# Optimization experiments

Measured on AMD Instinct MI355X. Metric: run time of the kernel, lower is better.

## Reference

```python
import math
import jax, jax.numpy as jnp
import numpy as np

B, S, H, NH = 4, 2048, 1024, 16
HD = H // NH
SCALE = math.sqrt(H)  # module divides by sqrt(hidden_dim), not sqrt(head_dim)


def setup_inputs() -> dict:
    key = jax.random.key(0)
    ks = jax.random.split(key, 9)
    lim = 1.0 / math.sqrt(H)
    def lin(kw, kb):
        W = jax.random.uniform(kw, (H, H), jnp.float32, -lim, lim)
        b = jax.random.uniform(kb, (H,), jnp.float32, -lim, lim)
        return W, b
    Wq, bq = lin(ks[0], ks[1])
    Wk, bk = lin(ks[2], ks[3])
    Wv, bv = lin(ks[4], ks[5])
    Wo, bo = lin(ks[6], ks[7])
    hidden_states = jax.random.normal(ks[8], (B, S, H), jnp.float32)
    masks = jnp.ones((B, S), jnp.float32)
    return {"hidden_states": hidden_states, "masks": masks,
            "Wq": Wq, "bq": bq, "Wk": Wk, "bk": bk,
            "Wv": Wv, "bv": bv, "Wo": Wo, "bo": bo}


def reference(hidden_states, masks, Wq, bq, Wk, bk, Wv, bv, Wo, bo):
    bsz, msl, hdim = hidden_states.shape
    def proj(W, b):
        # [b, s, h] -> [b, nh, s, hd]
        y = hidden_states @ W.T + b
        return y.reshape(bsz, msl, NH, HD).transpose(0, 2, 1, 3)
    q = proj(Wq, bq)
    k = proj(Wk, bk)
    v = proj(Wv, bv)
    scores = jnp.einsum('bnqd,bnkd->bnqk', q, k) / SCALE
    # mask outer product: [b,1,q,k], zero where either token is padded
    m2 = (masks[:, None, :, None] * masks[:, None, None, :])
    scores = jnp.where(m2 == 0, jnp.float32(-1e12), scores)
    attn = jax.nn.softmax(scores, axis=-1)
    ctx = jnp.einsum('bnqk,bnkd->bnqd', attn, v)
    ctx = ctx.transpose(0, 2, 1, 3).reshape(bsz, msl, hdim)
    return ctx @ Wo.T + bo
```

## Files before the change

kernel.cpp:

```cpp
#include <hip/hip_runtime.h>
#include <hip/hip_bf16.h>
#include <stdint.h>

typedef unsigned short u16;
typedef __attribute__((ext_vector_type(4))) float f32x4;
typedef __attribute__((ext_vector_type(8))) short bf16x8;
typedef __attribute__((ext_vector_type(4))) unsigned int u32x4;

#define GLL16(src, dst) __builtin_amdgcn_global_load_lds( \
    (const __attribute__((address_space(1))) void*)(src), \
    (__attribute__((address_space(3))) void*)(dst), 16, 0, 0)

static __device__ __forceinline__ u16 f2bf(float x) {
    uint32_t u = __builtin_bit_cast(uint32_t, x);
    u += 0x7fffu + ((u >> 16) & 1u);
    return (u16)(u >> 16);
}

static __device__ __forceinline__ uint32_t cvtpk(float lo, float hi) {
    uint32_t r;
    asm("v_cvt_pk_bf16_f32 %0, %1, %2" : "=v"(r) : "v"(lo), "v"(hi));
    return r;
}

__global__ __launch_bounds__(256) void cvt_f32_bf16(
        const float* __restrict__ in, u16* __restrict__ out, int n4) {
    int i = blockIdx.x * 256 + threadIdx.x;
    if (i >= n4) return;
    float4 v = ((const float4*)in)[i];
    ushort4 o;
    o.x = f2bf(v.x); o.y = f2bf(v.y); o.z = f2bf(v.z); o.w = f2bf(v.w);
    ((ushort4*)out)[i] = o;
}

__global__ __launch_bounds__(256) void cvt_w4(
        const float* __restrict__ s0, const float* __restrict__ s1,
        const float* __restrict__ s2, const float* __restrict__ s3,
        u16* __restrict__ dst) {
    int wsel = blockIdx.y;
    const float* s = (wsel == 0) ? s0 : (wsel == 1) ? s1 : (wsel == 2) ? s2 : s3;
    int i = blockIdx.x * 256 + threadIdx.x;
    float4 v = ((const float4*)s)[i];
    ushort4 o;
    o.x = f2bf(v.x); o.y = f2bf(v.y); o.z = f2bf(v.z); o.w = f2bf(v.w);
    ((ushort4*)(dst + (size_t)wsel * 1024 * 1024))[i] = o;
}

__global__ __launch_bounds__(256, 2) void gemm_qkv(
        const u16* __restrict__ A, const u16* __restrict__ W,
        const float* __restrict__ bq, const float* __restrict__ bk,
        const float* __restrict__ bv,
        u16* __restrict__ Qo, u16* __restrict__ Ko, u16* __restrict__ Vo) {
    __shared__ __align__(16) u16 As[2][128 * 32];
    __shared__ __align__(16) u16 Bs[2][128 * 32];
    const int tid = threadIdx.x;
    const int lane = tid & 63;
    const int w = tid >> 6, wm = w >> 1, wn = w & 1;
    const int l15 = lane & 15, l4 = lane >> 4;
    int v = (blockIdx.x & 7) * 192 + (blockIdx.x >> 3);
    int vy = v / 24, vx = v - vy * 24;
    const int m0 = vy * 128, n0 = vx * 128;
    const float SC2 = 0.03125f * 1.44269504088896f;

    f32x4 acc[4][4];
#pragma unroll
    for (int i = 0; i < 4; i++)
#pragma unroll
        for (int j = 0; j < 4; j++) acc[i][j] = f32x4{0.f, 0.f, 0.f, 0.f};

#define QKV_STAGE(buf, kt) do {                                            \
    _Pragma("unroll")                                                      \
    for (int i_ = 0; i_ < 2; i_++) {                                       \
        int c_ = tid + i_ * 256;                                           \
        int row_ = c_ >> 2, slot_ = c_ & 3;                                \
        int cc_ = slot_ ^ ((row_ >> 1) & 3);                               \
        GLL16(A + (size_t)(m0 + row_) * 1024 + (kt) + cc_ * 8, As[buf] + c_ * 8); \
    }                                                                      \
    _Pragma("unroll")                                                      \
    for (int i_ = 0; i_ < 2; i_++) {                                       \
        int c_ = tid + i_ * 256;                                           \
        int row_ = c_ >> 2, slot_ = c_ & 3;                                \
        int cc_ = slot_ ^ ((row_ >> 1) & 3);                               \
        GLL16(W + (size_t)(n0 + row_) * 1024 + (kt) + cc_ * 8, Bs[buf] + c_ * 8); \
    }                                                                      \
} while (0)

    QKV_STAGE(0, 0);
    __syncthreads();

    for (int kt = 0; kt < 1024; kt += 32) {
        const int cur = (kt >> 5) & 1;
        if (kt != 992) QKV_STAGE(cur ^ 1, kt + 32);

        bf16x8 af[4], bfr[4];
#pragma unroll
        for (int i = 0; i < 4; i++) {
            int row = wm * 64 + i * 16 + l15;
            int slot = l4 ^ ((row >> 1) & 3);
            af[i] = *(const bf16x8*)(As[cur] + row * 32 + slot * 8);
        }
#pragma unroll
        for (int j = 0; j < 4; j++) {
            int row = wn * 64 + j * 16 + l15;
            int slot = l4 ^ ((row >> 1) & 3);
            bfr[j] = *(const bf16x8*)(Bs[cur] + row * 32 + slot * 8);
        }
#pragma unroll
        for (int i = 0; i < 4; i++)
#pragma unroll
            for (int j = 0; j < 4; j++)
                acc[i][j] = __builtin_amdgcn_mfma_f32_16x16x32_bf16(af[i], bfr[j], acc[i][j], 0, 0, 0);
        __syncthreads();
    }
#undef QKV_STAGE

#pragma unroll
    for (int j = 0; j < 4; j++) {
        int col = n0 + wn * 64 + j * 16 + l15;
        int sel = col >> 10;
        float bvv = (sel == 0) ? bq[col] : (sel == 1) ? bk[col - 1024] : bv[col - 2048];
#pragma unroll
        for (int i = 0; i < 4; i++) {
            int rowb = m0 + wm * 64 + i * 16 + l4 * 4;
            if (sel == 0) {
#pragma unroll
                for (int r = 0; r < 4; r++)
                    Qo[(size_t)(rowb + r) * 1024 + col] = f2bf((acc[i][j][r] + bvv) * SC2);
            } else if (sel == 1) {
#pragma unroll
                for (int r = 0; r < 4; r++)
                    Ko[(size_t)(rowb + r) * 1024 + (col - 1024)] = f2bf(acc[i][j][r] + bvv);
            } else {
                int cc = col - 2048;
                int bb = rowb >> 11;
                int sp = ((m0 + wm * 64) & 2047) + (i >> 1) * 32 + l4 * 8 + (i & 1) * 4;
                int hh = cc >> 6, dd = cc & 63;
                ushort4 o;
                o.x = f2bf(acc[i][j][0] + bvv);
                o.y = f2bf(acc[i][j][1] + bvv);
                o.z = f2bf(acc[i][j][2] + bvv);
                o.w = f2bf(acc[i][j][3] + bvv);
                *(ushort4*)(Vo + ((size_t)((bb * 16 + hh) * 64 + dd)) * 2048 + sp) = o;
            }
        }
    }
}

__global__ __launch_bounds__(256, 2) void gemm_o(
        const u16* __restrict__ A, const u16* __restrict__ W,
        const float* __restrict__ bias, float* __restrict__ out) {
    __shared__ __align__(16) u16 As[2][128 * 32];
    __shared__ __align__(16) u16 Bs[2][128 * 32];
    const int tid = threadIdx.x;
    const int lane = tid & 63;
    const int w = tid >> 6, wm = w >> 1, wn = w & 1;
    const int l15 = lane & 15, l4 = lane >> 4;
    int v = (blockIdx.x & 7) * 64 + (blockIdx.x >> 3);
    int vy = v >> 3, vx = v & 7;
    const int m0 = vy * 128, n0 = vx * 128;

    f32x4 acc[4][4];
#pragma unroll
    for (int i = 0; i < 4; i++)
#pragma unroll
        for (int j = 0; j < 4; j++) acc[i][j] = f32x4{0.f, 0.f, 0.f, 0.f};

#define O_STAGE(buf, kt) do {                                              \
    _Pragma("unroll")                                                      \
    for (int i_ = 0; i_ < 2; i_++) {                                       \
        int c_ = tid + i_ * 256;                                           \
        int row_ = c_ >> 2, slot_ = c_ & 3;                                \
        int cc_ = slot_ ^ ((row_ >> 1) & 3);                               \
        GLL16(A + (size_t)(m0 + row_) * 1024 + (kt) + cc_ * 8, As[buf] + c_ * 8); \
    }                                                                      \
    _Pragma("unroll")                                                      \
    for (int i_ = 0; i_ < 2; i_++) {                                       \
        int c_ = tid + i_ * 256;                                           \
        int row_ = c_ >> 2, slot_ = c_ & 3;                                \
        int cc_ = slot_ ^ ((row_ >> 1) & 3);                               \
        GLL16(W + (size_t)(n0 + row_) * 1024 + (kt) + cc_ * 8, Bs[buf] + c_ * 8); \
    }                                                                      \
} while (0)

    O_STAGE(0, 0);
    __syncthreads();

    for (int kt = 0; kt < 1024; kt += 32) {
        const int cur = (kt >> 5) & 1;
        if (kt != 992) O_STAGE(cur ^ 1, kt + 32);

        bf16x8 af[4], bfr[4];
#pragma unroll
        for (int i = 0; i < 4; i++) {
            int row = wm * 64 + i * 16 + l15;
            int slot = l4 ^ ((row >> 1) & 3);
            af[i] = *(const bf16x8*)(As[cur] + row * 32 + slot * 8);
        }
#pragma unroll
        for (int j = 0; j < 4; j++) {
            int row = wn * 64 + j * 16 + l15;
            int slot = l4 ^ ((row >> 1) & 3);
            bfr[j] = *(const bf16x8*)(Bs[cur] + row * 32 + slot * 8);
        }
#pragma unroll
        for (int i = 0; i < 4; i++)
#pragma unroll
            for (int j = 0; j < 4; j++)
                acc[i][j] = __builtin_amdgcn_mfma_f32_16x16x32_bf16(af[i], bfr[j], acc[i][j], 0, 0, 0);
        __syncthreads();
    }
#undef O_STAGE

#pragma unroll
    for (int j = 0; j < 4; j++) {
        int col = n0 + wn * 64 + j * 16 + l15;
        float bvv = bias[col];
#pragma unroll
        for (int i = 0; i < 4; i++) {
            int rowb = m0 + wm * 64 + i * 16 + l4 * 4;
#pragma unroll
            for (int r = 0; r < 4; r++)
                out[(size_t)(rowb + r) * 1024 + col] = acc[i][j][r] + bvv;
        }
    }
}

__global__ __launch_bounds__(256, 3) void attn_fused(
        const u16* __restrict__ Q, const u16* __restrict__ K,
        const u16* __restrict__ Vt, const float* __restrict__ mask,
        u16* __restrict__ ctx) {
    __shared__ __align__(16) u16 Ks[2][64 * 64];
    __shared__ __align__(16) u16 Vs[2][64 * 64];

    const int tid = threadIdx.x, lane = tid & 63, w = tid >> 6;
    const int l15 = lane & 15, l4 = lane >> 4;
    const int bid = blockIdx.x;
    const int inner = bid >> 3;
    const int bh = ((inner >> 4) << 3) | (bid & 7);
    const int b = bh >> 4, h = bh & 15;
    const int qw = (inner & 15) * 128 + w * 32;
    const float THR2 = 8.0f;

    const u16* Qg = Q + (size_t)b * 2048 * 1024 + h * 64;
    const u16* Kg = K + (size_t)b * 2048 * 1024 + h * 64;
    const u16* Vg = Vt + (size_t)bh * 64 * 2048;
    const float* mp = mask + b * 2048;

    bool anym;
    {
        bool bad = false;
#pragma unroll
        for (int i = 0; i < 8; i++) {
            float4 a = ((const float4*)mp)[lane * 8 + i];
            bad |= (a.x == 0.f) | (a.y == 0.f) | (a.z == 0.f) | (a.w == 0.f);
        }
        anym = (__ballot(bad) != 0ull);
    }

#define STAGE_KV(buf, kvbase) do {                                         \
    _Pragma("unroll")                                                      \
    for (int i_ = 0; i_ < 2; i_++) {                                       \
        int c_ = tid + i_ * 256;                                           \
        int row_ = c_ >> 3, slot_ = c_ & 7;                                \
        int cc_ = slot_ ^ (row_ & 7);                                      \
        GLL16(Kg + (size_t)((kvbase) + row_) * 1024 + cc_ * 8, Ks[buf] + c_ * 8); \
    }                                                                      \
    _Pragma("unroll")                                                      \
    for (int i_ = 0; i_ < 2; i_++) {                                       \
        int c_ = tid + i_ * 256;                                           \
        int row_ = c_ >> 3, slot_ = c_ & 7;                                \
        int cc_ = slot_ ^ (row_ & 7);                                      \
        GLL16(Vg + (size_t)row_ * 2048 + (kvbase) + cc_ * 8, Vs[buf] + c_ * 8); \
    }                                                                      \
} while (0)

    bf16x8 qfr[2][2];
#pragma unroll
    for (int qi = 0; qi < 2; qi++)
#pragma unroll
        for (int kf = 0; kf < 2; kf++)
            qfr[qi][kf] = *(const bf16x8*)(Qg + (size_t)(qw + qi * 16 + l15) * 1024 + kf * 32 + l4 * 8);

    float mq01[2];
#pragma unroll
    for (int qi = 0; qi < 2; qi++)
        mq01[qi] = (mp[qw + qi * 16 + l15] != 0.f) ? 1.f : 0.f;

    float m_run[2] = {0.f, 0.f};
    f32x4 acc_l[2];
    f32x4 oaccT[4][2];
#pragma unroll
    for (int qi = 0; qi < 2; qi++) acc_l[qi] = f32x4{0.f, 0.f, 0.f, 0.f};
#pragma unroll
    for (int df = 0; df < 4; df++)
#pragma unroll
        for (int qi = 0; qi < 2; qi++) oaccT[df][qi] = f32x4{0.f, 0.f, 0.f, 0.f};

    const u32x4 ones4 = u32x4{0x3F803F80u, 0x3F803F80u, 0x3F803F80u, 0x3F803F80u};
    const bf16x8 ones = __builtin_bit_cast(bf16x8, ones4);

    STAGE_KV(0, 0);

    for (int it = 0; it < 32; ++it) {
        const int cur = it & 1;
        const int kv0 = it * 64;

        if (it != 31) {
            STAGE_KV(cur ^ 1, kv0 + 64);
            asm volatile("s_waitcnt vmcnt(4)" ::: "memory");
        } else {
            asm volatile("s_waitcnt vmcnt(0)" ::: "memory");
        }
        __builtin_amdgcn_s_barrier();

        bf16x8 kfr[4][2];
#pragma unroll
        for (int kvf = 0; kvf < 4; kvf++)
#pragma unroll
            for (int kf = 0; kf < 2; kf++) {
                int row = kvf * 16 + l15;
                int slot = (kf * 4 + l4) ^ (row & 7);
                kfr[kvf][kf] = *(const bf16x8*)(Ks[cur] + row * 64 + slot * 8);
            }
        f32x4 p[4][2];
#pragma unroll
        for (int kvf = 0; kvf < 4; kvf++)
#pragma unroll
            for (int qi = 0; qi < 2; qi++) p[kvf][qi] = f32x4{0.f, 0.f, 0.f, 0.f};
        __builtin_amdgcn_s_setprio(1);
#pragma unroll
        for (int kvf = 0; kvf < 4; kvf++)
#pragma unroll
            for (int qi = 0; qi < 2; qi++)
#pragma unroll
                for (int kf = 0; kf < 2; kf++)
                    p[kvf][qi] = __builtin_amdgcn_mfma_f32_16x16x32_bf16(kfr[kvf][kf], qfr[qi][kf], p[kvf][qi], 0, 0, 0);
        __builtin_amdgcn_s_setprio(0);

        bf16x8 vfr[4][2];
#pragma unroll
        for (int df = 0; df < 4; df++)
#pragma unroll
            for (int kf = 0; kf < 2; kf++) {
                int row = df * 16 + l15;
                int slot = (kf * 4 + l4) ^ (row & 7);
                vfr[df][kf] = *(const bf16x8*)(Vs[cur] + row * 64 + slot * 8);
            }

        if (anym) {
            float4 mkv[4];
#pragma unroll
            for (int kvf = 0; kvf < 4; kvf++)
                mkv[kvf] = ((const float4*)(mp + kv0))[kvf * 4 + l4];
#pragma unroll
            for (int qi = 0; qi < 2; qi++)
#pragma unroll
                for (int kvf = 0; kvf < 4; kvf++)
#pragma unroll
                    for (int r = 0; r < 4; r++) {
                        float bb = (mkv[kvf][r] != 0.f) ? 0.f : -1e12f;
                        p[kvf][qi][r] = __builtin_fmaf(p[kvf][qi][r], mq01[qi], bb);
                    }
        }

        float t[2];
#pragma unroll
        for (int qi = 0; qi < 2; qi++) {
            float a0 = fmaxf(fmaxf(p[0][qi][0], p[0][qi][1]), fmaxf(p[0][qi][2], p[0][qi][3]));
            float a1 = fmaxf(fmaxf(p[1][qi][0], p[1][qi][1]), fmaxf(p[1][qi][2], p[1][qi][3]));
            float a2 = fmaxf(fmaxf(p[2][qi][0], p[2][qi][1]), fmaxf(p[2][qi][2], p[2][qi][3]));
            float a3 = fmaxf(fmaxf(p[3][qi][0], p[3][qi][1]), fmaxf(p[3][qi][2], p[3][qi][3]));
            t[qi] = fmaxf(fmaxf(a0, a1), fmaxf(a2, a3));
        }
        if (!__all((t[0] <= m_run[0] + THR2) && (t[1] <= m_run[1] + THR2))) {
#pragma unroll
            for (int qi = 0; qi < 2; qi++) {
                float tt = fmaxf(t[qi], __shfl_xor(t[qi], 16));
                tt = fmaxf(tt, __shfl_xor(tt, 32));
                float mn = fmaxf(m_run[qi], tt);
                float sc = __builtin_amdgcn_exp2f(m_run[qi] - mn);
                m_run[qi] = mn;
                acc_l[qi] *= sc;
#pragma unroll
                for (int df = 0; df < 4; df++) oaccT[df][qi] *= sc;
            }
        }
        if (__all((m_run[0] == 0.f) & (m_run[1] == 0.f))) {
#pragma unroll
            for (int qi = 0; qi < 2; qi++)
#pragma unroll
                for (int kvf = 0; kvf < 4; kvf++)
#pragma unroll
                    for (int r = 0; r < 4; r++)
                        p[kvf][qi][r] = __builtin_amdgcn_exp2f(p[kvf][qi][r]);
        } else {
#pragma unroll
            for (int qi = 0; qi < 2; qi++)
#pragma unroll
                for (int kvf = 0; kvf < 4; kvf++)
#pragma unroll
                    for (int r = 0; r < 4; r++)
                        p[kvf][qi][r] = __builtin_amdgcn_exp2f(p[kvf][qi][r] - m_run[qi]);
        }

        bf16x8 pb[2][2];
#pragma unroll
        for (int qi = 0; qi < 2; qi++)
#pragma unroll
            for (int kf = 0; kf < 2; kf++) {
                u32x4 tq;
                tq.x = cvtpk(p[2 * kf][qi][0], p[2 * kf][qi][1]);
                tq.y = cvtpk(p[2 * kf][qi][2], p[2 * kf][qi][3]);
                tq.z = cvtpk(p[2 * kf + 1][qi][0], p[2 * kf + 1][qi][1]);
                tq.w = cvtpk(p[2 * kf + 1][qi][2], p[2 * kf + 1][qi][3]);
                pb[qi][kf] = __builtin_bit_cast(bf16x8, tq);
            }

        __builtin_amdgcn_s_setprio(1);
#pragma unroll
        for (int df = 0; df < 4; df++)
#pragma unroll
            for (int qi = 0; qi < 2; qi++)
#pragma unroll
                for (int kf = 0; kf < 2; kf++)
                    oaccT[df][qi] = __builtin_amdgcn_mfma_f32_16x16x32_bf16(vfr[df][kf], pb[qi][kf], oaccT[df][qi], 0, 0, 0);
#pragma unroll
        for (int qi = 0; qi < 2; qi++)
#pragma unroll
            for (int kf = 0; kf < 2; kf++)
                acc_l[qi] = __builtin_amdgcn_mfma_f32_16x16x32_bf16(ones, pb[qi][kf], acc_l[qi], 0, 0, 0);
        __builtin_amdgcn_s_setprio(0);

        __builtin_amdgcn_s_barrier();
    }

#pragma unroll
    for (int qi = 0; qi < 2; qi++) {
        float rl = 1.0f / acc_l[qi][0];
        int tok = qw + qi * 16 + l15;
#pragma unroll
        for (int df = 0; df < 4; df++) {
            uint2 o;
            o.x = cvtpk(oaccT[df][qi][0] * rl, oaccT[df][qi][1] * rl);
            o.y = cvtpk(oaccT[df][qi][2] * rl, oaccT[df][qi][3] * rl);
            *(uint2*)(ctx + (size_t)(b * 2048 + tok) * 1024 + h * 64 + df * 16 + l4 * 4) = o;
        }
    }
#undef STAGE_KV
}

extern "C" void kernel_launch(void* const* d_in, const int* in_sizes, int n_in,
                              void* d_out, int out_size, void* d_ws, size_t ws_size,
                              hipStream_t stream) {
    const float* hs    = (const float*)d_in[0];
    const float* masks = (const float*)d_in[1];
    const float* Wq = (const float*)d_in[2];
    const float* bq = (const float*)d_in[3];
    const float* Wk = (const float*)d_in[4];
    const float* bk = (const float*)d_in[5];
    const float* Wv = (const float*)d_in[6];
    const float* bv = (const float*)d_in[7];
    const float* Wo = (const float*)d_in[8];
    const float* bo = (const float*)d_in[9];

    const int NT = 4 * 2048;
    const int H = 1024;

    u16* hs_b = (u16*)d_ws;
    u16* w_b  = hs_b + (size_t)NT * H;
    u16* wo_b = w_b + (size_t)3 * H * H;
    u16* Qb   = w_b + (size_t)4 * H * H;
    u16* Kb   = Qb + (size_t)NT * H;
    u16* Vtb  = Kb + (size_t)NT * H;
    u16* Cb   = hs_b;

    cvt_f32_bf16<<<NT * H / 1024, 256, 0, stream>>>(hs, hs_b, NT * H / 4);
    cvt_w4<<<dim3(H * H / 1024, 4), 256, 0, stream>>>(Wq, Wk, Wv, Wo, w_b);

    gemm_qkv<<<1536, 256, 0, stream>>>(hs_b, w_b, bq, bk, bv, Qb, Kb, Vtb);

    attn_fused<<<1024, 256, 0, stream>>>(Qb, Kb, Vtb, masks, Cb);

    gemm_o<<<512, 256, 0, stream>>>(Cb, wo_b, bo, (float*)d_out);
}
```

Measured before the change: 202.4 us.

## Unify projection GEMMs into 256x128x64-tiled 8-wave kernel and simplify attention sync

Result: slower. 217.1 us (+7.3%).

```diff
diff --git a/kernel.cpp b/kernel.cpp
--- a/kernel.cpp
+++ b/kernel.cpp
@@ -46,183 +46,146 @@
     ((ushort4*)(dst + (size_t)wsel * 1024 * 1024))[i] = o;
 }
 
-__global__ __launch_bounds__(256, 2) void gemm_qkv(
+template <int MODE>
+__global__ __launch_bounds__(512, 2) void gemm2(
         const u16* __restrict__ A, const u16* __restrict__ W,
-        const float* __restrict__ bq, const float* __restrict__ bk,
-        const float* __restrict__ bv,
-        u16* __restrict__ Qo, u16* __restrict__ Ko, u16* __restrict__ Vo) {
-    __shared__ __align__(16) u16 As[2][128 * 32];
-    __shared__ __align__(16) u16 Bs[2][128 * 32];
+        const float* __restrict__ b0, const float* __restrict__ b1,
+        const float* __restrict__ b2,
+        void* __restrict__ o0, void* __restrict__ o1, void* __restrict__ o2) {
+    __shared__ __align__(16) u16 As[2][256 * 64];
+    __shared__ __align__(16) u16 Bs[2][128 * 64];
     const int tid = threadIdx.x;
     const int lane = tid & 63;
-    const int w = tid >> 6, wm = w >> 1, wn = w & 1;
+    const int w = tid >> 6, wm = w >> 2, wn = w & 3;
     const int l15 = lane & 15, l4 = lane >> 4;
-    int v = (blockIdx.x & 7) * 192 + (blockIdx.x >> 3);
-    int vy = v / 24, vx = v - vy * 24;
-    const int m0 = vy * 128, n0 = vx * 128;
+    constexpr int NXB = (MODE == 0) ? 24 : 8;
+    constexpr int CPX = (MODE == 0) ? 96 : 32;
+    int v = (blockIdx.x & 7) * CPX + (blockIdx.x >> 3);
+    int vy = v / NXB, vx = v - vy * NXB;
+    const int m0 = vy * 256, n0 = vx * 128;
     const float SC2 = 0.03125f * 1.44269504088896f;
 
-    f32x4 acc[4][4];
-#pragma unroll
-    for (int i = 0; i < 4; i++)
-#pragma unroll
-        for (int j = 0; j < 4; j++) acc[i][j] = f32x4{0.f, 0.f, 0.f, 0.f};
-
-#define QKV_STAGE(buf, kt) do {                                            \
-    _Pragma("unroll")                                                      \
-    for (int i_ = 0; i_ < 2; i_++) {                                       \
-        int c_ = tid + i_ * 256;                                           \
-        int row_ = c_ >> 2, slot_ = c_ & 3;                                \
-        int cc_ = slot_ ^ ((row_ >> 1) & 3);                               \
-        GLL16(A + (size_t)(m0 + row_) * 1024 + (kt) + cc_ * 8, As[buf] + c_ * 8); \
-    }                                                                      \
-    _Pragma("unroll")                                                      \
-    for (int i_ = 0; i_ < 2; i_++) {                                       \
-        int c_ = tid + i_ * 256;                                           \
-        int row_ = c_ >> 2, slot_ = c_ & 3;                                \
-        int cc_ = slot_ ^ ((row_ >> 1) & 3);                               \
-        GLL16(W + (size_t)(n0 + row_) * 1024 + (kt) + cc_ * 8, Bs[buf] + c_ * 8); \
-    }                                                                      \
+#define G2_STAGE_A(buf, kt, i) do {                                        \
+    int c_ = tid + (i) * 512;                                              \
+    int row_ = c_ >> 3, slot_ = c_ & 7;                                    \
+    int cc_ = slot_ ^ (row_ & 7);                                          \
+    GLL16(A + (size_t)(m0 + row_) * 1024 + (kt) + cc_ * 8, As[buf] + c_ * 8); \
 } while (0)
-
-    QKV_STAGE(0, 0);
-    __syncthreads();
-
-    for (int kt = 0; kt < 1024; kt += 32) {
-        const int cur = (kt >> 5) & 1;
-        if (kt != 992) QKV_STAGE(cur ^ 1, kt + 32);
-
-        bf16x8 af[4], bfr[4];
-#pragma unroll
-        for (int i = 0; i < 4; i++) {
-            int row = wm * 64 + i * 16 + l15;
-            int slot = l4 ^ ((row >> 1) & 3);
-            af[i] = *(const bf16x8*)(As[cur] + row * 32 + slot * 8);
-        }
-#pragma unroll
-        for (int j = 0; j < 4; j++) {
-            int row = wn * 64 + j * 16 + l15;
-            int slot = l4 ^ ((row >> 1) & 3);
-            bfr[j] = *(const bf16x8*)(Bs[cur] + row * 32 + slot * 8);
-        }
-#pragma unroll
-        for (int i = 0; i < 4; i++)
-#pragma unroll
-            for (int j = 0; j < 4; j++)
-                acc[i][j] = __builtin_amdgcn_mfma_f32_16x16x32_bf16(af[i], bfr[j], acc[i][j], 0, 0, 0);
-        __syncthreads();
+#define G2_STAGE_B(buf, kt, i) do {                                        \
+    int c_ = tid + (i) * 512;                                              \
+    int row_ = c_ >> 3, slot_ = c_ & 7;                                    \
+    int cc_ = slot_ ^ (row_ & 7);                                          \
+    GLL16(W + (size_t)(n0 + row_) * 1024 + (kt) + cc_ * 8, Bs[buf] + c_ * 8); \
+} while (0)
+
+    f32x4 acc[8][2];
+#pragma unroll
+    for (int mi = 0; mi < 8; mi++)
+#pragma unroll
+        for (int nj = 0; nj < 2; nj++) acc[mi][nj] = f32x4{0.f, 0.f, 0.f, 0.f};
+
+    G2_STAGE_A(0, 0, 0); G2_STAGE_A(0, 0, 1); G2_STAGE_A(0, 0, 2); G2_STAGE_A(0, 0, 3);
+    G2_STAGE_B(0, 0, 0); G2_STAGE_B(0, 0, 1);
+
+    for (int t = 0; t < 16; ++t) {
+        const int cur = t & 1, nxt = cur ^ 1;
+        const int ktn = (t + 1) * 64;
+
+        asm volatile("s_waitcnt vmcnt(0)" ::: "memory");
+        __builtin_amdgcn_s_barrier();
+        __builtin_amdgcn_sched_barrier(0);
+
+        bf16x8 bfr[2][2];
+#pragma unroll
+        for (int nj = 0; nj < 2; nj++)
+#pragma unroll
+            for (int kh = 0; kh < 2; kh++) {
+                int row = wn * 32 + nj * 16 + l15;
+                int slot = (kh * 4 + l4) ^ (row & 7);
+                bfr[nj][kh] = *(const bf16x8*)(Bs[cur] + row * 64 + slot * 8);
+            }
+
+#pragma unroll
+        for (int p = 0; p < 4; p++) {
+            bf16x8 af[2][2];
+#pragma unroll
+            for (int m2 = 0; m2 < 2; m2++)
+#pragma unroll
+                for (int kh = 0; kh < 2; kh++) {
+                    int mi = p * 2 + m2;
+                    int row = wm * 128 + mi * 16 + l15;
+                    int slot = (kh * 4 + l4) ^ (row & 7);
+                    af[m2][kh] = *(const bf16x8*)(As[cur] + row * 64 + slot * 8);
+                }
+            if (t != 15) {
+                if (p == 0) { G2_STAGE_A(nxt, ktn, 0); G2_STAGE_A(nxt, ktn, 1); }
+                else if (p == 1) { G2_STAGE_A(nxt, ktn, 2); G2_STAGE_A(nxt, ktn, 3); }
+                else if (p == 2) { G2_STAGE_B(nxt, ktn, 0); G2_STAGE_B(nxt, ktn, 1); }
+            }
+            __builtin_amdgcn_s_barrier();
+            __builtin_amdgcn_s_setprio(1);
+#pragma unroll
+            for (int m2 = 0; m2 < 2; m2++)
+#pragma unroll
+                for (int nj = 0; nj < 2; nj++)
+#pragma unroll
+                    for (int kh = 0; kh < 2; kh++)
+                        acc[p * 2 + m2][nj] = __builtin_amdgcn_mfma_f32_16x16x32_bf16(
+                            af[m2][kh], bfr[nj][kh], acc[p * 2 + m2][nj], 0, 0, 0);
+            __builtin_amdgcn_s_setprio(0);
+            __builtin_amdgcn_s_barrier();
+        }
     }
-#undef QKV_STAGE
-
-#pragma unroll
-    for (int j = 0; j < 4; j++) {
-        int col = n0 + wn * 64 + j * 16 + l15;
-        int sel = col >> 10;
-        float bvv = (sel == 0) ? bq[col] : (sel == 1) ? bk[col - 1024] : bv[col - 2048];
-#pragma unroll
-        for (int i = 0; i < 4; i++) {
-            int rowb = m0 + wm * 64 + i * 16 + l4 * 4;
-            if (sel == 0) {
+
+#pragma unroll
+    for (int nj = 0; nj < 2; nj++) {
+        int col = n0 + wn * 32 + nj * 16 + l15;
+        if (MODE == 1) {
+            float bvv = b0[col];
+            float* out = (float*)o0;
+#pragma unroll
+            for (int mi = 0; mi < 8; mi++) {
+                int rowb = m0 + wm * 128 + mi * 16 + l4 * 4;
 #pragma unroll
                 for (int r = 0; r < 4; r++)
-                    Qo[(size_t)(rowb + r) * 1024 + col] = f2bf((acc[i][j][r] + bvv) * SC2);
-            } else if (sel == 1) {
-#pragma unroll
-                for (int r = 0; r < 4; r++)
-                    Ko[(size_t)(rowb + r) * 1024 + (col - 1024)] = f2bf(acc[i][j][r] + bvv);
-            } else {
-                int cc = col - 2048;
-                int bb = rowb >> 11;
-                int sp = ((m0 + wm * 64) & 2047) + (i >> 1) * 32 + l4 * 8 + (i & 1) * 4;
-                int hh = cc >> 6, dd = cc & 63;
-                ushort4 o;
-                o.x = f2bf(acc[i][j][0] + bvv);
-                o.y = f2bf(acc[i][j][1] + bvv);
-                o.z = f2bf(acc[i][j][2] + bvv);
-                o.w = f2bf(acc[i][j][3] + bvv);
-                *(ushort4*)(Vo + ((size_t)((bb * 16 + hh) * 64 + dd)) * 2048 + sp) = o;
+                    out[(size_t)(rowb + r) * 1024 + col] = acc[mi][nj][r] + bvv;
+            }
+        } else {
+            int sel = col >> 10;
+            float bvv = (sel == 0) ? b0[col] : (sel == 1) ? b1[col - 1024] : b2[col - 2048];
+#pragma unroll
+            for (int mi = 0; mi < 8; mi++) {
+                int rowb = m0 + wm * 128 + mi * 16 + l4 * 4;
+                if (sel == 0) {
+                    u16* out = (u16*)o0;
+#pragma unroll
+                    for (int r = 0; r < 4; r++)
+                        out[(size_t)(rowb + r) * 1024 + col] = f2bf((acc[mi][nj][r] + bvv) * SC2);
+                } else if (sel == 1) {
+                    u16* out = (u16*)o1;
+#pragma unroll
+                    for (int r = 0; r < 4; r++)
+                        out[(size_t)(rowb + r) * 1024 + (col - 1024)] = f2bf(acc[mi][nj][r] + bvv);
+                } else {
+                    u16* out = (u16*)o2;
+                    int cc2 = col - 2048;
+                    int g64 = m0 + wm * 128 + (mi >> 2) * 64;
+                    int i64 = mi & 3;
+                    int bb = g64 >> 11;
+                    int sp = (g64 & 2047) + (i64 >> 1) * 32 + l4 * 8 + (i64 & 1) * 4;
+                    int hh = cc2 >> 6, dd = cc2 & 63;
+                    ushort4 o;
+                    o.x = f2bf(acc[mi][nj][0] + bvv);
+                    o.y = f2bf(acc[mi][nj][1] + bvv);
+                    o.z = f2bf(acc[mi][nj][2] + bvv);
+                    o.w = f2bf(acc[mi][nj][3] + bvv);
+                    *(ushort4*)(out + ((size_t)((bb * 16 + hh) * 64 + dd)) * 2048 + sp) = o;
+                }
             }
         }
     }
-}
-
-__global__ __launch_bounds__(256, 2) void gemm_o(
-        const u16* __restrict__ A, const u16* __restrict__ W,
-        const float* __restrict__ bias, float* __restrict__ out) {
-    __shared__ __align__(16) u16 As[2][128 * 32];
-    __shared__ __align__(16) u16 Bs[2][128 * 32];
-    const int tid = threadIdx.x;
-    const int lane = tid & 63;
-    const int w = tid >> 6, wm = w >> 1, wn = w & 1;
-    const int l15 = lane & 15, l4 = lane >> 4;
-    int v = (blockIdx.x & 7) * 64 + (blockIdx.x >> 3);
-    int vy = v >> 3, vx = v & 7;
-    const int m0 = vy * 128, n0 = vx * 128;
-
-    f32x4 acc[4][4];
-#pragma unroll
-    for (int i = 0; i < 4; i++)
-#pragma unroll
-        for (int j = 0; j < 4; j++) acc[i][j] = f32x4{0.f, 0.f, 0.f, 0.f};
-
-#define O_STAGE(buf, kt) do {                                              \
-    _Pragma("unroll")                                                      \
-    for (int i_ = 0; i_ < 2; i_++) {                                       \
-        int c_ = tid + i_ * 256;                                           \
-        int row_ = c_ >> 2, slot_ = c_ & 3;                                \
-        int cc_ = slot_ ^ ((row_ >> 1) & 3);                               \
-        GLL16(A + (size_t)(m0 + row_) * 1024 + (kt) + cc_ * 8, As[buf] + c_ * 8); \
-    }                                                                      \
-    _Pragma("unroll")                                                      \
-    for (int i_ = 0; i_ < 2; i_++) {                                       \
-        int c_ = tid + i_ * 256;                                           \
-        int row_ = c_ >> 2, slot_ = c_ & 3;                                \
-        int cc_ = slot_ ^ ((row_ >> 1) & 3);                               \
-        GLL16(W + (size_t)(n0 + row_) * 1024 + (kt) + cc_ * 8, Bs[buf] + c_ * 8); \
-    }                                                                      \
-} while (0)
-
-    O_STAGE(0, 0);
-    __syncthreads();
-
-    for (int kt = 0; kt < 1024; kt += 32) {
-        const int cur = (kt >> 5) & 1;
-        if (kt != 992) O_STAGE(cur ^ 1, kt + 32);
-
-        bf16x8 af[4], bfr[4];
-#pragma unroll
-        for (int i = 0; i < 4; i++) {
-            int row = wm * 64 + i * 16 + l15;
-            int slot = l4 ^ ((row >> 1) & 3);
-            af[i] = *(const bf16x8*)(As[cur] + row * 32 + slot * 8);
-        }
-#pragma unroll
-        for (int j = 0; j < 4; j++) {
-            int row = wn * 64 + j * 16 + l15;
-            int slot = l4 ^ ((row >> 1) & 3);
-            bfr[j] = *(const bf16x8*)(Bs[cur] + row * 32 + slot * 8);
-        }
-#pragma unroll
-        for (int i = 0; i < 4; i++)
-#pragma unroll
-            for (int j = 0; j < 4; j++)
-                acc[i][j] = __builtin_amdgcn_mfma_f32_16x16x32_bf16(af[i], bfr[j], acc[i][j], 0, 0, 0);
-        __syncthreads();
-    }
-#undef O_STAGE
-
-#pragma unroll
-    for (int j = 0; j < 4; j++) {
-        int col = n0 + wn * 64 + j * 16 + l15;
-        float bvv = bias[col];
-#pragma unroll
-        for (int i = 0; i < 4; i++) {
-            int rowb = m0 + wm * 64 + i * 16 + l4 * 4;
-#pragma unroll
-            for (int r = 0; r < 4; r++)
-                out[(size_t)(rowb + r) * 1024 + col] = acc[i][j][r] + bvv;
-        }
-    }
+#undef G2_STAGE_A
+#undef G2_STAGE_B
 }
 
 __global__ __launch_bounds__(256, 3) void attn_fused(
@@ -300,18 +263,13 @@
     const bf16x8 ones = __builtin_bit_cast(bf16x8, ones4);
 
     STAGE_KV(0, 0);
+    __syncthreads();
 
     for (int it = 0; it < 32; ++it) {
         const int cur = it & 1;
         const int kv0 = it * 64;
 
-        if (it != 31) {
-            STAGE_KV(cur ^ 1, kv0 + 64);
-            asm volatile("s_waitcnt vmcnt(4)" ::: "memory");
-        } else {
-            asm volatile("s_waitcnt vmcnt(0)" ::: "memory");
-        }
-        __builtin_amdgcn_s_barrier();
+        if (it != 31) STAGE_KV(cur ^ 1, kv0 + 64);
 
         bf16x8 kfr[4][2];
 #pragma unroll
@@ -336,16 +294,6 @@
                 for (int kf = 0; kf < 2; kf++)
                     p[kvf][qi] = __builtin_amdgcn_mfma_f32_16x16x32_bf16(kfr[kvf][kf], qfr[qi][kf], p[kvf][qi], 0, 0, 0);
         __builtin_amdgcn_s_setprio(0);
-
-        bf16x8 vfr[4][2];
-#pragma unroll
-        for (int df = 0; df < 4; df++)
-#pragma unroll
-            for (int kf = 0; kf < 2; kf++) {
-                int row = df * 16 + l15;
-                int slot = (kf * 4 + l4) ^ (row & 7);
-                vfr[df][kf] = *(const bf16x8*)(Vs[cur] + row * 64 + slot * 8);
-            }
 
         if (anym) {
             float4 mkv[4];
@@ -416,6 +364,16 @@
                 pb[qi][kf] = __builtin_bit_cast(bf16x8, tq);
             }
 
+        bf16x8 vfr[4][2];
+#pragma unroll
+        for (int df = 0; df < 4; df++)
+#pragma unroll
+            for (int kf = 0; kf < 2; kf++) {
+                int row = df * 16 + l15;
+                int slot = (kf * 4 + l4) ^ (row & 7);
+                vfr[df][kf] = *(const bf16x8*)(Vs[cur] + row * 64 + slot * 8);
+            }
+
         __builtin_amdgcn_s_setprio(1);
 #pragma unroll
         for (int df = 0; df < 4; df++)
@@ -431,7 +389,7 @@
                 acc_l[qi] = __builtin_amdgcn_mfma_f32_16x16x32_bf16(ones, pb[qi][kf], acc_l[qi], 0, 0, 0);
         __builtin_amdgcn_s_setprio(0);
 
-        __builtin_amdgcn_s_barrier();
+        __syncthreads();
     }
 
 #pragma unroll
@@ -477,9 +435,10 @@
     cvt_f32_bf16<<<NT * H / 1024, 256, 0, stream>>>(hs, hs_b, NT * H / 4);
     cvt_w4<<<dim3(H * H / 1024, 4), 256, 0, stream>>>(Wq, Wk, Wv, Wo, w_b);
 
-    gemm_qkv<<<1536, 256, 0, stream>>>(hs_b, w_b, bq, bk, bv, Qb, Kb, Vtb);
+    gemm2<0><<<768, 512, 0, stream>>>(hs_b, w_b, bq, bk, bv, Qb, Kb, Vtb);
 
     attn_fused<<<1024, 256, 0, stream>>>(Qb, Kb, Vtb, masks, Cb);
 
-    gemm_o<<<512, 256, 0, stream>>>(Cb, wo_b, bo, (float*)d_out);
-}
+    gemm2<1><<<256, 512, 0, stream>>>(Cb, wo_b, bo, nullptr, nullptr,
+                                      (void*)d_out, nullptr, nullptr);
+}
```
